# Optimization experiments

Measured on AMD Instinct MI355X. Metric: run time of the kernel, lower is better.

Reference implementation:

```python
import jax, jax.numpy as jnp
import numpy as np
from jax import lax

D3 = 48      # manifold_dim * 3
M = 512      # mem_slots
H = 256      # slot_dim
K = 32       # topk
IN = 1024    # input_dim
ODE_HID = 128
ODE_STEPS = 2
ODE_DT = 0.5
TEMP = 1.0   # temperature buffer
LN_EPS = 1e-5


def _ln(x, g, b):
    m = jnp.mean(x, axis=-1, keepdims=True)
    v = jnp.mean(jnp.square(x - m), axis=-1, keepdims=True)
    return (x - m) * lax.rsqrt(v + LN_EPS) * g + b


def setup_inputs() -> dict:
    key = jax.random.key(0)
    ks = jax.random.split(key, 12)
    s_in = 1.0 / np.sqrt(IN)
    s_h = 1.0 / np.sqrt(H)
    s_d3 = 1.0 / np.sqrt(D3)
    s_ode = 1.0 / np.sqrt(ODE_HID)
    return {
        "x": jax.random.normal(ks[0], (16, 2048, IN), jnp.float32),
        "w1": jax.random.uniform(ks[1], (IN, D3), jnp.float32, -s_in, s_in),
        "b1": jnp.zeros((D3,), jnp.float32),
        "g1": jnp.ones((D3,), jnp.float32),
        "be1": jnp.zeros((D3,), jnp.float32),
        "wa": jax.random.uniform(ks[2], (D3, ODE_HID), jnp.float32, -s_d3, s_d3),
        "ba": jnp.zeros((ODE_HID,), jnp.float32),
        "wb": jax.random.uniform(ks[3], (ODE_HID, D3), jnp.float32, -s_ode, s_ode),
        "bb": jnp.zeros((D3,), jnp.float32),
        "mem": jax.random.normal(ks[4], (M, H), jnp.float32),
        "pos": jax.random.normal(ks[5], (M, 16, 3), jnp.float32),
        "curv": jax.random.normal(ks[6], (M, 16), jnp.float32),
        "alpha": jnp.float32(0.1),
        "wo": jax.random.uniform(ks[7], (H, IN), jnp.float32, -s_h, s_h),
        "bo": jnp.zeros((IN,), jnp.float32),
        "go": jnp.ones((IN,), jnp.float32),
        "beo": jnp.zeros((IN,), jnp.float32),
    }


def reference(x, w1, b1, g1, be1, wa, ba, wb, bb, mem, pos, curv, alpha, wo, bo, go, beo):
    # manifold projection: Linear -> LayerNorm -> GELU, viewed as (B,S,D,3)
    h = jax.nn.gelu(_ln(x @ w1 + b1, g1, be1), approximate=False)  # (B,S,48)
    # ODE evolution (2 fixed steps over the flattened manifold coords)
    for _ in range(ODE_STEPS):
        dx = jnp.tanh(h @ wa + ba) @ wb + bb
        h = h + ODE_DT * dx
    # attend: query side is detached in the original
    q = lax.stop_gradient(h)                       # (B,S,48)
    mem_pos = pos.reshape(M, -1)                   # (512,48)
    # squared pairwise L2: ||q||^2 - 2 q.m + ||m||^2
    dist = (jnp.sum(q * q, axis=-1, keepdims=True)
            - 2.0 * jnp.einsum('bsd,md->bsm', q, mem_pos)
            + jnp.sum(mem_pos * mem_pos, axis=-1))
    dist = jnp.maximum(dist, 0.0) / max(TEMP, 1e-6)
    curv_w = jnp.exp(-alpha * jnp.linalg.norm(curv, axis=-1))  # (512,)
    dist = dist * curv_w[None, None, :]
    # topk smallest distances
    neg_top, itop = lax.top_k(-dist, K)            # (B,S,K)
    w = jax.nn.softmax(neg_top, axis=-1)           # softmax(-dtop)
    slots = mem[itop]                              # (B,S,K,256) gather
    attended = jnp.einsum('bsk,bskh->bsh', w, slots)
    # output projection: Linear -> LayerNorm -> GELU
    return jax.nn.gelu(_ln(attended @ wo + bo, go, beo), approximate=False)
```

## Files before the change

### kernel.cpp

```cpp
#include <hip/hip_runtime.h>
#include <stdint.h>

typedef unsigned short u16;
typedef __attribute__((ext_vector_type(4))) short short4v;
typedef __attribute__((ext_vector_type(8))) short short8v;
typedef __attribute__((ext_vector_type(4))) float f32x4;
typedef __attribute__((address_space(1))) void gv;
typedef __attribute__((address_space(3))) void lv;

#define NTOK 32768

__device__ __forceinline__ float bf2f(u16 u){ return __uint_as_float(((uint32_t)u)<<16); }
__device__ __forceinline__ u16 f2bf(float f){
  uint32_t u = __float_as_uint(f);
  u += 0x7FFFu + ((u>>16)&1u);
  return (u16)(u>>16);
}
__device__ __forceinline__ void hilo(float v, u16& h, u16& l){
  h = f2bf(v);
  l = f2bf(v - bf2f(h));
}
__device__ __forceinline__ void tsplit(float v, u16& h, u16& l){
  uint32_t b = __float_as_uint(v);
  h = (u16)(b >> 16);
  float lf = v - __uint_as_float(b & 0xFFFF0000u);
  l = (u16)(__float_as_uint(lf) >> 16);
}
__device__ __forceinline__ void tpack8(float4 a, float4 b, short8v& hi, short8v& lo){
  float v[8] = {a.x,a.y,a.z,a.w,b.x,b.y,b.z,b.w};
  #pragma unroll
  for (int i=0;i<8;++i){ u16 h,l; tsplit(v[i],h,l); hi[i]=(short)h; lo[i]=(short)l; }
}
__device__ __forceinline__ float gelu_f(float v){ return 0.5f*v*(1.0f + erff(v*0.70710678118654752440f)); }
__device__ __forceinline__ float gelu_t(float x){
  float u = 0.7978845608028654f*(x + 0.044715f*x*x*x);
  float t = 1.0f - 2.0f/(__expf(2.0f*u) + 1.0f);
  return 0.5f*x*(1.0f + t);
}
__device__ __forceinline__ float tanh_f(float x){ return 1.0f - 2.0f/(__expf(2.0f*x)+1.0f); }

__global__ __launch_bounds__(256) void k_prep(
    const float* __restrict__ w1, const float* __restrict__ wa, const float* __restrict__ wb,
    const float* __restrict__ pos, const float* __restrict__ curv,
    const float* __restrict__ mem, const float* __restrict__ wo,
    const float* __restrict__ alpha,
    u16* __restrict__ w1s, u16* __restrict__ wah, u16* __restrict__ wbh,
    float2* __restrict__ mnw,
    u16* __restrict__ memb, u16* __restrict__ woB, u16* __restrict__ posB)
{
  int i = blockIdx.x*256 + threadIdx.x;
  if (i < 49152){ int n = i>>10, k = i&1023; u16 h,l; hilo(w1[k*48+n], h, l);
                  w1s[i] = h; w1s[49152+i] = l; return; }
  i -= 49152;
  if (i < 8192){ int u = i>>6, d = i&63; float v = (d<48) ? wa[d*128+u] : 0.f;
                 u16 h,l; hilo(v,h,l); wah[i] = h; wah[8192+i] = l; return; }
  i -= 8192;
  if (i < 6144){ int n = i>>7, u = i&127; u16 h,l; hilo(wb[u*48+n], h, l);
                 wbh[i] = h; wbh[6144+i] = l; return; }
  i -= 6144;
  if (i < 512){
    float s = 0.f;
    #pragma unroll
    for (int d=0; d<48; ++d){ float v = pos[i*48+d]; s += v*v; }
    float c2 = 0.f;
    #pragma unroll
    for (int d=0; d<16; ++d){ float v = curv[i*16+d]; c2 += v*v; }
    mnw[i] = make_float2(s, expf(-alpha[0]*sqrtf(c2)));
    return;
  }
  i -= 512;
  if (i < 131072){ memb[i] = f2bf(mem[i]); return; }
  i -= 131072;
  if (i < 262144){
    int e = i & 7, ln = (i>>3)&63, n = (i>>9)&15, cpq = (i>>13)&3, kt = i>>15;
    int col = cpq*256 + n*16 + (ln & 15);
    int k   = kt*32 + (ln >> 4)*8 + e;
    woB[i] = f2bf(wo[k*1024 + col]);
    return;
  }
  i -= 262144;
  if (i < 32768){
    int e = i & 7, ln = (i>>3)&63, n = (i>>9)&31, ks = i>>14;
    int slot = n*16 + (ln&15);
    int d = ks*32 + (ln>>4)*8 + e;
    float v = (d < 48) ? pos[slot*48 + d] : 0.f;
    u16 h,l; hilo(v,h,l);
    posB[i] = h; posB[32768+i] = l;
  }
}

__global__ __launch_bounds__(256, 2) void k_proj(
    const float* __restrict__ x, const u16* __restrict__ w1s,
    const float* __restrict__ b1, const float* __restrict__ g1, const float* __restrict__ be1,
    float* __restrict__ hout)
{
  extern __shared__ char dynp[];
  float* xsl = (float*)dynp;
  u16*   bsl = (u16*)(dynp + 49152);

  const int tid = threadIdx.x;
  const int lane = tid & 63, w = tid >> 6;
  const int l15 = lane & 15, l4 = lane >> 4;
  const int bm = blockIdx.x;
  const int arow = w*16 + l15;

  f32x4 acc[3];
  #pragma unroll
  for (int n=0; n<3; ++n) acc[n] = (f32x4){0.f,0.f,0.f,0.f};

  auto stage_x = [&](float* dst, int kt){
    #pragma unroll
    for (int j=0; j<4; ++j){
      int idx = (j*4 + w)*64 + lane;
      int row = idx >> 4, q = idx & 15;
      int chunk = q >> 1, half = q & 1;
      const float* src = x + (size_t)(bm*64 + row)*1024 + kt*64 + ((chunk ^ (row & 7))*8 + half*4);
      __builtin_amdgcn_global_load_lds((gv*)src, (lv*)(dst + (j*4 + w)*256), 16, 0, 0);
    }
  };
  auto stage_b = [&](u16* dst, int kt){
    #pragma unroll
    for (int j=0; j<3; ++j){
      int idx = (j*4 + w)*64 + lane;
      int hl = (idx >= 384) ? 1 : 0;
      int rr = idx - hl*384;
      int row = rr >> 3, ch = rr & 7;
      const u16* src = w1s + hl*49152 + (size_t)row*1024 + kt*64 + ((ch ^ (row & 7))*8);
      __builtin_amdgcn_global_load_lds((gv*)src, (lv*)(dst + (j*4 + w)*512), 16, 0, 0);
    }
  };
  auto mfma_from = [&](const float* xb, const u16* bb){
    #pragma unroll
    for (int kq=0; kq<2; ++kq){
      int chunk = kq*4 + l4;
      int phys = chunk ^ (arow & 7);
      const float* xa = xb + arow*64 + phys*8;
      float4 a0 = *(const float4*)xa;
      float4 a1 = *(const float4*)(xa + 4);
      short8v ah, al; tpack8(a0, a1, ah, al);
      #pragma unroll
      for (int n=0; n<3; ++n){
        int brow = n*16 + l15;
        int bcx = chunk ^ (brow & 7);
        short8v bh = *(const short8v*)(bb + brow*64 + bcx*8);
        short8v bl = *(const short8v*)(bb + 3072 + brow*64 + bcx*8);
        acc[n] = __builtin_amdgcn_mfma_f32_16x16x32_bf16(ah, bh, acc[n], 0, 0, 0);
        acc[n] = __builtin_amdgcn_mfma_f32_16x16x32_bf16(ah, bl, acc[n], 0, 0, 0);
        acc[n] = __builtin_amdgcn_mfma_f32_16x16x32_bf16(al, bh, acc[n], 0, 0, 0);
      }
    }
  };

  float* x0 = xsl;         float* x1 = xsl + 4096;  float* x2 = xsl + 8192;
  u16*   b0 = bsl;         u16*   b1b = bsl + 6144;

  stage_b(b0, 0);
  stage_x(x0, 0);
  stage_x(x1, 1);

  float* xc = x0; float* xn = x1; float* xn2 = x2;
  u16* bc = b0;  u16* bn = b1b;

  for (int kt = 0; kt < 15; ++kt){
    asm volatile("s_waitcnt vmcnt(4)" ::: "memory");
    __builtin_amdgcn_s_barrier();
    __builtin_amdgcn_sched_barrier(0);
    mfma_from(xc, bc);
    stage_b(bn, kt + 1);
    if (kt < 14) stage_x(xn2, kt + 2);
    { float* t = xc; xc = xn; xn = xn2; xn2 = t; }
    { u16* t = bc; bc = bn; bn = t; }
  }
  asm volatile("s_waitcnt vmcnt(0)" ::: "memory");
  __builtin_amdgcn_s_barrier();
  __builtin_amdgcn_sched_barrier(0);
  mfma_from(xc, bc);

  float b1r[3], g1r[3], e1r[3];
  #pragma unroll
  for (int n=0; n<3; ++n){ int c = n*16 + l15; b1r[n] = b1[c]; g1r[n] = g1[c]; e1r[n] = be1[c]; }
  #pragma unroll
  for (int r=0; r<4; ++r){
    float a0 = acc[0][r] + b1r[0];
    float a1 = acc[1][r] + b1r[1];
    float a2 = acc[2][r] + b1r[2];
    float s1 = a0+a1+a2;
    float s2 = a0*a0 + a1*a1 + a2*a2;
    #pragma unroll
    for (int m=1; m<16; m<<=1){ s1 += __shfl_xor(s1, m); s2 += __shfl_xor(s2, m); }
    float mean = s1 * (1.f/48.f);
    float var  = s2 * (1.f/48.f) - mean*mean;
    float rs = rsqrtf(var + 1e-5f);
    int row = bm*64 + w*16 + l4*4 + r;
    float* hb = hout + (size_t)row*48;
    hb[l15]      = gelu_f((a0-mean)*rs*g1r[0] + e1r[0]);
    hb[16+l15]   = gelu_f((a1-mean)*rs*g1r[1] + e1r[1]);
    hb[32+l15]   = gelu_f((a2-mean)*rs*g1r[2] + e1r[2]);
  }
}

__global__ __launch_bounds__(256) void k_ode(
    const float* __restrict__ hin,
    const u16* __restrict__ wah, const u16* __restrict__ wbh,
    const float* __restrict__ ba, const float* __restrict__ bb,
    float* __restrict__ hout, float* __restrict__ q2b)
{
  extern __shared__ u16 sm[];
  u16* t_hi = sm;
  u16* t_lo = sm + 16384;
  u16* h_hi = sm + 32768;
  u16* h_lo = sm + 40960;
  float* hscr = (float*)sm;

  const int tid = threadIdx.x;
  const int lane = tid & 63, w = tid >> 6;
  const int l15 = lane & 15, l4 = lane >> 4;
  const int bm = blockIdx.x;

  float4 hv4[6];
  #pragma unroll
  for (int it=0; it<6; ++it){
    int q = it*256 + tid;
    int row = q/12, c4 = q - row*12;
    hv4[it] = *(const float4*)(hin + (size_t)(bm*128 + row)*48 + c4*4);
  }
  #pragma unroll
  for (int it=0; it<6; ++it){
    int q = it*256 + tid;
    int row = q/12, c4 = q - row*12;
    *(float4*)&hscr[row*48 + c4*4] = hv4[it];
    float4 v = hv4[it];
    u16 h0,l0,h1,l1,h2,l2,h3,l3;
    tsplit(v.x,h0,l0); tsplit(v.y,h1,l1); tsplit(v.z,h2,l2); tsplit(v.w,h3,l3);
    int off = row*64 + ((c4>>1) ^ (row & 7))*8 + (c4 & 1)*4;
    short4v hv = {(short)h0,(short)h1,(short)h2,(short)h3};
    short4v lv = {(short)l0,(short)l1,(short)l2,(short)l3};
    *(short4v*)&h_hi[off] = hv;
    *(short4v*)&h_lo[off] = lv;
  }
  {
    int row = tid >> 1, ch = 6 + (tid & 1);
    int off = row*64 + (ch ^ (row & 7))*8;
    uint4 z = {0u,0u,0u,0u};
    *(uint4*)&h_hi[off] = z;
    *(uint4*)&h_lo[off] = z;
  }
  __syncthreads();

  float hreg[2][3][4];
  #pragma unroll
  for (int m=0; m<2; ++m)
    #pragma unroll
    for (int n=0; n<3; ++n)
      #pragma unroll
      for (int r=0; r<4; ++r)
        hreg[m][n][r] = hscr[(w*32 + m*16 + l4*4 + r)*48 + n*16 + l15];
  __syncthreads();

  float ba_r[8], bb_r[3];
  #pragma unroll
  for (int n=0; n<8; ++n) ba_r[n] = ba[n*16 + l15];
  #pragma unroll
  for (int n=0; n<3; ++n) bb_r[n] = bb[n*16 + l15];

  for (int s=0; s<2; ++s){
    f32x4 at[2][8];
    #pragma unroll
    for (int m=0; m<2; ++m)
      #pragma unroll
      for (int n=0; n<8; ++n) at[m][n] = (f32x4){0.f,0.f,0.f,0.f};
    #pragma unroll
    for (int kq=0; kq<2; ++kq){
      short8v ah[2], al[2];
      #pragma unroll
      for (int m=0; m<2; ++m){
        int arow = w*32 + m*16 + l15;
        int ac = (kq*4 + l4) ^ (arow & 7);
        ah[m] = *(const short8v*)&h_hi[arow*64 + ac*8];
        al[m] = *(const short8v*)&h_lo[arow*64 + ac*8];
      }
      #pragma unroll
      for (int n=0; n<8; ++n){
        const u16* bp = wah + (n*16 + l15)*64 + kq*32 + l4*8;
        short8v bh = *(const short8v*)bp;
        short8v bl = *(const short8v*)(bp + 8192);
        #pragma unroll
        for (int m=0; m<2; ++m){
          at[m][n] = __builtin_amdgcn_mfma_f32_16x16x32_bf16(ah[m], bh, at[m][n], 0, 0, 0);
          at[m][n] = __builtin_amdgcn_mfma_f32_16x16x32_bf16(ah[m], bl, at[m][n], 0, 0, 0);
          at[m][n] = __builtin_amdgcn_mfma_f32_16x16x32_bf16(al[m], bh, at[m][n], 0, 0, 0);
        }
      }
    }
    #pragma unroll
    for (int m=0; m<2; ++m)
      #pragma unroll
      for (int n=0; n<8; ++n)
        #pragma unroll
        for (int r=0; r<4; ++r){
          float tv = tanh_f(at[m][n][r] + ba_r[n]);
          u16 th, tl; tsplit(tv, th, tl);
          int row = w*32 + m*16 + l4*4 + r;
          int col = n*16 + l15;
          int c = col >> 3;
          int phys = (c & 8) | ((c & 7) ^ (row & 7));
          int off = row*128 + phys*8 + (col & 7);
          t_hi[off] = th; t_lo[off] = tl;
        }
    __syncthreads();
    f32x4 ad[2][3];
    #pragma unroll
    for (int m=0; m<2; ++m)
      #pragma unroll
      for (int n=0; n<3; ++n) ad[m][n] = (f32x4){0.f,0.f,0.f,0.f};
    #pragma unroll
    for (int kq=0; kq<4; ++kq){
      short8v ah[2], al[2];
      #pragma unroll
      for (int m=0; m<2; ++m){
        int arow = w*32 + m*16 + l15;
        int c = kq*4 + l4;
        int phys = (c & 8) | ((c & 7) ^ (arow & 7));
        ah[m] = *(const short8v*)&t_hi[arow*128 + phys*8];
        al[m] = *(const short8v*)&t_lo[arow*128 + phys*8];
      }
      #pragma unroll
      for (int n=0; n<3; ++n){
        const u16* bp = wbh + (n*16 + l15)*128 + kq*32 + l4*8;
        short8v bh = *(const short8v*)bp;
        short8v bl = *(const short8v*)(bp + 6144);
        #pragma unroll
        for (int m=0; m<2; ++m){
          ad[m][n] = __builtin_amdgcn_mfma_f32_16x16x32_bf16(ah[m], bh, ad[m][n], 0, 0, 0);
          ad[m][n] = __builtin_amdgcn_mfma_f32_16x16x32_bf16(ah[m], bl, ad[m][n], 0, 0, 0);
          ad[m][n] = __builtin_amdgcn_mfma_f32_16x16x32_bf16(al[m], bh, ad[m][n], 0, 0, 0);
        }
      }
    }
    #pragma unroll
    for (int m=0; m<2; ++m)
      #pragma unroll
      for (int n=0; n<3; ++n)
        #pragma unroll
        for (int r=0; r<4; ++r)
          hreg[m][n][r] += 0.5f*(ad[m][n][r] + bb_r[n]);
    if (s == 0){
      #pragma unroll
      for (int m=0; m<2; ++m)
        #pragma unroll
        for (int n=0; n<3; ++n)
          #pragma unroll
          for (int r=0; r<4; ++r){
            u16 hh, hl2; tsplit(hreg[m][n][r], hh, hl2);
            int row = w*32 + m*16 + l4*4 + r;
            int col = n*16 + l15;
            int off = row*64 + ((col>>3) ^ (row & 7))*8 + (col & 7);
            h_hi[off] = hh; h_lo[off] = hl2;
          }
      __syncthreads();
    }
  }
  #pragma unroll
  for (int m=0; m<2; ++m){
    #pragma unroll
    for (int r=0; r<4; ++r){
      size_t row = (size_t)(bm*128 + w*32 + m*16 + l4*4 + r);
      #pragma unroll
      for (int n=0; n<3; ++n)
        hout[row*64 + n*16 + l15] = hreg[m][n][r];
      hout[row*64 + 48 + l15] = 0.f;
      float s2 = hreg[m][0][r]*hreg[m][0][r] + hreg[m][1][r]*hreg[m][1][r] + hreg[m][2][r]*hreg[m][2][r];
      #pragma unroll
      for (int msk=1; msk<16; msk<<=1) s2 += __shfl_xor(s2, msk);
      if (l15 == 0) q2b[row] = s2;
    }
  }
}

__global__ __launch_bounds__(256, 4) void k_sel(
    const float* __restrict__ h, const float* __restrict__ q2b,
    const u16* __restrict__ posB, const float2* __restrict__ mnw,
    uint32_t* __restrict__ glist)
{
  __shared__ __align__(16) uint32_t tokKeys[2*4*528];

  const int tid = threadIdx.x;
  const int lane = tid & 63, w = tid >> 6;
  const int g = w >> 1, s = w & 1;
  const int l15 = lane & 15, l4 = lane >> 4;
  const int bm = blockIdx.x;

  const float* hrow = h + (size_t)(bm*32 + g*16 + l15)*64;
  float4 x0 = *(const float4*)(hrow + l4*8);
  float4 x1 = *(const float4*)(hrow + l4*8 + 4);
  float4 x2 = *(const float4*)(hrow + 32 + l4*8);
  float4 x3 = *(const float4*)(hrow + 32 + l4*8 + 4);
  short8v ah0, al0, ah1, al1;
  tpack8(x0, x1, ah0, al0);
  tpack8(x2, x3, ah1, al1);

  float4 q2v = *(const float4*)(q2b + bm*32 + g*16 + l4*4);
  float q2a[4] = {q2v.x, q2v.y, q2v.z, q2v.w};

  uint32_t kk[16][4];
  #pragma unroll
  for (int n=0; n<16; ++n){
    const u16* pb = posB + (size_t)(s*16 + n)*512 + lane*8;
    short8v bh0 = *(const short8v*)(pb);
    short8v bl0 = *(const short8v*)(pb + 32768);
    short8v bh1 = *(const short8v*)(pb + 16384);
    short8v bl1 = *(const short8v*)(pb + 49152);
    f32x4 acc = (f32x4){0.f,0.f,0.f,0.f};
    acc = __builtin_amdgcn_mfma_f32_16x16x32_bf16(ah0, bh0, acc, 0, 0, 0);
    acc = __builtin_amdgcn_mfma_f32_16x16x32_bf16(ah0, bl0, acc, 0, 0, 0);
    acc = __builtin_amdgcn_mfma_f32_16x16x32_bf16(al0, bh0, acc, 0, 0, 0);
    acc = __builtin_amdgcn_mfma_f32_16x16x32_bf16(ah1, bh1, acc, 0, 0, 0);
    acc = __builtin_amdgcn_mfma_f32_16x16x32_bf16(ah1, bl1, acc, 0, 0, 0);
    acc = __builtin_amdgcn_mfma_f32_16x16x32_bf16(al1, bh1, acc, 0, 0, 0);
    const int slot = s*256 + n*16 + l15;
    float2 mw = mnw[slot];
    #pragma unroll
    for (int r=0; r<4; ++r){
      float dd = fmaxf(q2a[r] + mw.x - 2.f*acc[r], 0.f) * mw.y;
      kk[n][r] = (__float_as_uint(dd) & 0xFFFFFE00u) | (uint32_t)slot;
    }
  }

  const int gbase = g*2112;
  const unsigned long long ltmask = (lane == 63) ? 0x7FFFFFFFFFFFFFFFull : ((1ull << lane) - 1ull);
  #pragma unroll
  for (int r=0; r<4; ++r){
    __syncthreads();
    #pragma unroll
    for (int n=0; n<16; ++n)
      tokKeys[gbase + l4*528 + s*256 + n*16 + l15] = kk[n][r];
    __syncthreads();
    uint32_t key8[2][8];
    #pragma unroll
    for (int j=0; j<2; ++j){
      *(uint4*)&key8[j][0] = *(const uint4*)&tokKeys[gbase + (s*2+j)*528 + lane*8];
      *(uint4*)&key8[j][4] = *(const uint4*)&tokKeys[gbase + (s*2+j)*528 + lane*8 + 4];
    }
    uint32_t p[2] = {0u,0u};
    for (int b=30; b>=0; --b){
      #pragma unroll
      for (int j=0; j<2; ++j){
        uint32_t c = p[j] | (1u<<b);
        int cnt = 0;
        #pragma unroll
        for (int i=0; i<8; ++i) cnt += (int)__popcll(__ballot(key8[j][i] < c));
        if (cnt <= 31) p[j] = c;
      }
    }
    #pragma unroll
    for (int j=0; j<2; ++j){
      size_t tok = (size_t)bm*32 + g*16 + (s*2+j)*4 + r;
      int base = 0;
      #pragma unroll
      for (int i=0; i<8; ++i){
        unsigned long long bal = __ballot(key8[j][i] <= p[j]);
        if (key8[j][i] <= p[j]){
          int idx = base + (int)__popcll(bal & ltmask);
          glist[tok*32 + idx] = key8[j][i];
        }
        base += (int)__popcll(bal);
      }
    }
  }
}

__global__ __launch_bounds__(256) void k_attend(
    const uint32_t* __restrict__ glist, const u16* __restrict__ memb,
    u16* __restrict__ att)
{
  const int lane = threadIdx.x & 63, w = threadIdx.x >> 6;
  const size_t tok = (size_t)blockIdx.x*4 + w;
  uint32_t lk[32];
  const uint4* lp = (const uint4*)(glist + tok*32);
  #pragma unroll
  for (int q=0; q<8; ++q) *(uint4*)&lk[q*4] = lp[q];
  uint32_t km = lk[0];
  #pragma unroll
  for (int i=1; i<32; ++i) km = min(km, lk[i]);
  const float dminf = __uint_as_float(km & 0xFFFFFE00u);

  float den = 0.f, a0=0.f, a1=0.f, a2=0.f, a3=0.f;
  #pragma unroll
  for (int i=0; i<32; ++i){
    float dk = __uint_as_float(lk[i] & 0xFFFFFE00u);
    int slot = (int)(lk[i] & 511u);
    float wg = __expf(dminf - dk);
    den += wg;
    uint2 mv = ((const uint2*)(memb + (size_t)slot*256))[lane];
    a0 += wg*bf2f((u16)(mv.x & 0xFFFFu));
    a1 += wg*bf2f((u16)(mv.x >> 16));
    a2 += wg*bf2f((u16)(mv.y & 0xFFFFu));
    a3 += wg*bf2f((u16)(mv.y >> 16));
  }
  float inv = 1.f/den;
  uint32_t o0 = (uint32_t)f2bf(a0*inv) | ((uint32_t)f2bf(a1*inv) << 16);
  uint32_t o1 = (uint32_t)f2bf(a2*inv) | ((uint32_t)f2bf(a3*inv) << 16);
  ((uint2*)(att + tok*256))[lane] = make_uint2(o0, o1);
}

__global__ __launch_bounds__(1024, 4) void k_out(
    const u16* __restrict__ A, const u16* __restrict__ woB, const float* __restrict__ bo,
    const float* __restrict__ go, const float* __restrict__ beo, float* __restrict__ out)
{
  __shared__ u16 Asl[64*256];
  __shared__ float red1[16*65];
  __shared__ float red2[16*65];

  const int tid = threadIdx.x;
  const int lane = tid & 63, w = tid >> 6;
  const int l15 = lane & 15, l4 = lane >> 4;
  const int bm = blockIdx.x;

  #pragma unroll
  for (int j=0; j<2; ++j){
    int idx = j*1024 + tid;
    int row = idx >> 5, ch = idx & 31;
    int gc = (ch & 24) | ((ch & 7) ^ (row & 7));
    uint4 v = *(const uint4*)(A + (size_t)(bm*64 + row)*256 + gc*8);
    *(uint4*)&Asl[row*256 + ch*8] = v;
  }
  __syncthreads();

  f32x4 acc[4][4];
  #pragma unroll
  for (int m=0; m<4; ++m)
    #pragma unroll
    for (int n=0; n<4; ++n) acc[m][n] = (f32x4){0.f,0.f,0.f,0.f};

  #pragma unroll
  for (int kt=0; kt<8; ++kt){
    const int c = kt*4 + l4;
    short8v af[4];
    #pragma unroll
    for (int m=0; m<4; ++m){
      int arow = m*16 + l15;
      int aphys = (c & 24) | ((c & 7) ^ (arow & 7));
      af[m] = *(const short8v*)&Asl[arow*256 + aphys*8];
    }
    const u16* bbase = woB + ((size_t)kt*64 + w*4)*512 + lane*8;
    #pragma unroll
    for (int n=0; n<4; ++n){
      short8v bf = *(const short8v*)(bbase + n*512);
      #pragma unroll
      for (int m=0; m<4; ++m)
        acc[m][n] = __builtin_amdgcn_mfma_f32_16x16x32_bf16(af[m], bf, acc[m][n], 0, 0, 0);
    }
  }

  float bor[4];
  #pragma unroll
  for (int n=0; n<4; ++n) bor[n] = bo[w*64 + n*16 + l15];

  float s1[4][4], s2[4][4];
  #pragma unroll
  for (int m=0; m<4; ++m)
    #pragma unroll
    for (int r=0; r<4; ++r){ s1[m][r] = 0.f; s2[m][r] = 0.f; }
  #pragma unroll
  for (int m=0; m<4; ++m)
    #pragma unroll
    for (int n=0; n<4; ++n)
      #pragma unroll
      for (int r=0; r<4; ++r){
        float v = acc[m][n][r] + bor[n];
        acc[m][n][r] = v;
        s1[m][r] += v; s2[m][r] += v*v;
      }
  #pragma unroll
  for (int m=0; m<4; ++m)
    #pragma unroll
    for (int r=0; r<4; ++r){
      #pragma unroll
      for (int msk=1; msk<16; msk<<=1){
        s1[m][r] += __shfl_xor(s1[m][r], msk);
        s2[m][r] += __shfl_xor(s2[m][r], msk);
      }
    }
  if (l15 == 0){
    #pragma unroll
    for (int m=0; m<4; ++m)
      #pragma unroll
      for (int r=0; r<4; ++r){
        int t = m*16 + l4*4 + r;
        red1[w*65 + t] = s1[m][r];
        red2[w*65 + t] = s2[m][r];
      }
  }
  __syncthreads();

  float mean[4][4], rs[4][4];
  #pragma unroll
  for (int m=0; m<4; ++m)
    #pragma unroll
    for (int r=0; r<4; ++r){
      int t = m*16 + l4*4 + r;
      float a1 = red1[l15*65 + t];
      float a2 = red2[l15*65 + t];
      #pragma unroll
      for (int msk=1; msk<16; msk<<=1){
        a1 += __shfl_xor(a1, msk);
        a2 += __shfl_xor(a2, msk);
      }
      float mu = a1 * (1.f/1024.f);
      float var = a2 * (1.f/1024.f) - mu*mu;
      mean[m][r] = mu;
      rs[m][r] = rsqrtf(var + 1e-5f);
    }

  float gor[4], eor[4];
  #pragma unroll
  for (int n=0; n<4; ++n){
    int col = w*64 + n*16 + l15;
    gor[n] = go[col]; eor[n] = beo[col];
  }
  #pragma unroll
  for (int m=0; m<4; ++m)
    #pragma unroll
    for (int r=0; r<4; ++r){
      size_t row = (size_t)bm*64 + m*16 + l4*4 + r;
      float* op = out + row*1024 + w*64 + l15;
      float mu = mean[m][r], rv = rs[m][r];
      #pragma unroll
      for (int n=0; n<4; ++n){
        op[n*16] = gelu_t((acc[m][n][r] - mu)*rv*gor[n] + eor[n]);
      }
    }
}

extern "C" void kernel_launch(void* const* d_in, const int* in_sizes, int n_in,
                              void* d_out, int out_size, void* d_ws, size_t ws_size,
                              hipStream_t stream) {
  const float* x    = (const float*)d_in[0];
  const float* w1   = (const float*)d_in[1];
  const float* b1   = (const float*)d_in[2];
  const float* g1   = (const float*)d_in[3];
  const float* be1  = (const float*)d_in[4];
  const float* wa   = (const float*)d_in[5];
  const float* ba   = (const float*)d_in[6];
  const float* wb   = (const float*)d_in[7];
  const float* bb   = (const float*)d_in[8];
  const float* mem  = (const float*)d_in[9];
  const float* pos  = (const float*)d_in[10];
  const float* curv = (const float*)d_in[11];
  const float* alpha= (const float*)d_in[12];
  const float* wo   = (const float*)d_in[13];
  const float* bo   = (const float*)d_in[14];
  const float* go   = (const float*)d_in[15];
  const float* beo  = (const float*)d_in[16];
  float* out = (float*)d_out;

  char* ws = (char*)d_ws;
  size_t o = 0;
  auto take = [&](size_t b) -> char* { char* p = ws + o; o += (b + 255) & ~(size_t)255; return p; };
  char*  regA   = take(67108864);
  float* hbuf48 = (float*)regA;
  float* hbuf64 = (float*)(regA + 6291456);
  float* q2b    = (float*)(regA + 6291456 + 8388608);
  u16*   att    = (u16*)take(16777216);
  u16*   w1s    = (u16*)take(196608);
  u16*   wah    = (u16*)take(32768);
  u16*   wbh    = (u16*)take(24576);
  float2* mnw   = (float2*)take(4096);
  u16*   memb   = (u16*)take(262144);
  u16*   woB    = (u16*)take(524288);
  u16*   posB   = (u16*)take(131072);
  uint32_t* glist = (uint32_t*)take(4194304);

  hipFuncSetAttribute((const void*)k_ode, hipFuncAttributeMaxDynamicSharedMemorySize, 98304);
  hipFuncSetAttribute((const void*)k_proj, hipFuncAttributeMaxDynamicSharedMemorySize, 73728);

  k_prep<<<1914, 256, 0, stream>>>(w1, wa, wb, pos, curv, mem, wo, alpha,
                                   w1s, wah, wbh, mnw, memb, woB, posB);
  k_proj<<<512, 256, 73728, stream>>>(x, w1s, b1, g1, be1, hbuf48);
  k_ode<<<256, 256, 98304, stream>>>(hbuf48, wah, wbh, ba, bb, hbuf64, q2b);
  k_sel<<<1024, 256, 0, stream>>>(hbuf64, q2b, posB, mnw, glist);
  k_attend<<<8192, 256, 0, stream>>>(glist, memb, att);
  k_out<<<512, 1024, 0, stream>>>(att, woB, bo, go, beo, out);
  (void)in_sizes; (void)n_in; (void)out_size; (void)ws_size;
}
```

Measured before the change: 253.4 us.

## Halve ODE tile to 64 rows per block, drop syncs, use raw exp/rcp

The ODE kernel now processes 64 tokens per block instead of 128, with each wave owning 16 rows. Grid size doubles to 512 blocks and dynamic shared memory halves, which should improve occupancy and CU coverage. Each wave now reads back only the tanh and h rows it wrote itself, so the intra-step __syncthreads calls are removed. Separately, tanh, gelu_t and the softmax reciprocal use the hardware v_exp_f32/v_rcp_f32 instructions, trading a little accuracy for fewer ALU ops. Per-wave weight loads from global memory are now amortised over half as many rows.

```diff
diff --git a/kernel.cpp b/kernel.cpp
--- a/kernel.cpp
+++ b/kernel.cpp
@@ -31,13 +31,21 @@
   #pragma unroll
   for (int i=0;i<8;++i){ u16 h,l; tsplit(v[i],h,l); hi[i]=(short)h; lo[i]=(short)l; }
 }
+__device__ __forceinline__ float fexp2(float x){ float r; asm("v_exp_f32 %0, %1" : "=v"(r) : "v"(x)); return r; }
+__device__ __forceinline__ float frcp(float x){ float r; asm("v_rcp_f32 %0, %1" : "=v"(r) : "v"(x)); return r; }
+
 __device__ __forceinline__ float gelu_f(float v){ return 0.5f*v*(1.0f + erff(v*0.70710678118654752440f)); }
 __device__ __forceinline__ float gelu_t(float x){
-  float u = 0.7978845608028654f*(x + 0.044715f*x*x*x);
-  float t = 1.0f - 2.0f/(__expf(2.0f*u) + 1.0f);
-  return 0.5f*x*(1.0f + t);
-}
-__device__ __forceinline__ float tanh_f(float x){ return 1.0f - 2.0f/(__expf(2.0f*x)+1.0f); }
+  float p = x*(2.3022141f + 0.1029435f*x*x);
+  float e = fexp2(p);
+  float r = frcp(e + 1.0f);
+  return x*(1.0f - r);
+}
+__device__ __forceinline__ float tanh_f(float x){
+  float e = fexp2(2.8853901f*x);
+  float r = frcp(e + 1.0f);
+  return 1.0f - 2.0f*r;
+}
 
 __global__ __launch_bounds__(256) void k_prep(
     const float* __restrict__ w1, const float* __restrict__ wa, const float* __restrict__ wb,
@@ -207,9 +215,9 @@
 {
   extern __shared__ u16 sm[];
   u16* t_hi = sm;
-  u16* t_lo = sm + 16384;
-  u16* h_hi = sm + 32768;
-  u16* h_lo = sm + 40960;
+  u16* t_lo = sm + 8192;
+  u16* h_hi = sm + 16384;
+  u16* h_lo = sm + 20480;
   float* hscr = (float*)sm;
 
   const int tid = threadIdx.x;
@@ -217,15 +225,15 @@
   const int l15 = lane & 15, l4 = lane >> 4;
   const int bm = blockIdx.x;
 
-  float4 hv4[6];
-  #pragma unroll
-  for (int it=0; it<6; ++it){
+  float4 hv4[3];
+  #pragma unroll
+  for (int it=0; it<3; ++it){
     int q = it*256 + tid;
     int row = q/12, c4 = q - row*12;
-    hv4[it] = *(const float4*)(hin + (size_t)(bm*128 + row)*48 + c4*4);
-  }
-  #pragma unroll
-  for (int it=0; it<6; ++it){
+    hv4[it] = *(const float4*)(hin + (size_t)(bm*64 + row)*48 + c4*4);
+  }
+  #pragma unroll
+  for (int it=0; it<3; ++it){
     int q = it*256 + tid;
     int row = q/12, c4 = q - row*12;
     *(float4*)&hscr[row*48 + c4*4] = hv4[it];
@@ -238,7 +246,7 @@
     *(short4v*)&h_hi[off] = hv;
     *(short4v*)&h_lo[off] = lv;
   }
-  {
+  if (tid < 128){
     int row = tid >> 1, ch = 6 + (tid & 1);
     int off = row*64 + (ch ^ (row & 7))*8;
     uint4 z = {0u,0u,0u,0u};
@@ -247,14 +255,12 @@
   }
   __syncthreads();
 
-  float hreg[2][3][4];
-  #pragma unroll
-  for (int m=0; m<2; ++m)
-    #pragma unroll
-    for (int n=0; n<3; ++n)
-      #pragma unroll
-      for (int r=0; r<4; ++r)
-        hreg[m][n][r] = hscr[(w*32 + m*16 + l4*4 + r)*48 + n*16 + l15];
+  float hreg[3][4];
+  #pragma unroll
+  for (int n=0; n<3; ++n)
+    #pragma unroll
+    for (int r=0; r<4; ++r)
+      hreg[n][r] = hscr[(w*16 + l4*4 + r)*48 + n*16 + l15];
   __syncthreads();
 
   float ba_r[8], bb_r[3];
@@ -264,116 +270,87 @@
   for (int n=0; n<3; ++n) bb_r[n] = bb[n*16 + l15];
 
   for (int s=0; s<2; ++s){
-    f32x4 at[2][8];
-    #pragma unroll
-    for (int m=0; m<2; ++m)
-      #pragma unroll
-      for (int n=0; n<8; ++n) at[m][n] = (f32x4){0.f,0.f,0.f,0.f};
+    f32x4 at[8];
+    #pragma unroll
+    for (int n=0; n<8; ++n) at[n] = (f32x4){0.f,0.f,0.f,0.f};
     #pragma unroll
     for (int kq=0; kq<2; ++kq){
-      short8v ah[2], al[2];
-      #pragma unroll
-      for (int m=0; m<2; ++m){
-        int arow = w*32 + m*16 + l15;
-        int ac = (kq*4 + l4) ^ (arow & 7);
-        ah[m] = *(const short8v*)&h_hi[arow*64 + ac*8];
-        al[m] = *(const short8v*)&h_lo[arow*64 + ac*8];
-      }
+      const int arow = w*16 + l15;
+      int ac = (kq*4 + l4) ^ (arow & 7);
+      short8v ah = *(const short8v*)&h_hi[arow*64 + ac*8];
+      short8v al = *(const short8v*)&h_lo[arow*64 + ac*8];
       #pragma unroll
       for (int n=0; n<8; ++n){
         const u16* bp = wah + (n*16 + l15)*64 + kq*32 + l4*8;
         short8v bh = *(const short8v*)bp;
         short8v bl = *(const short8v*)(bp + 8192);
-        #pragma unroll
-        for (int m=0; m<2; ++m){
-          at[m][n] = __builtin_amdgcn_mfma_f32_16x16x32_bf16(ah[m], bh, at[m][n], 0, 0, 0);
-          at[m][n] = __builtin_amdgcn_mfma_f32_16x16x32_bf16(ah[m], bl, at[m][n], 0, 0, 0);
-          at[m][n] = __builtin_amdgcn_mfma_f32_16x16x32_bf16(al[m], bh, at[m][n], 0, 0, 0);
-        }
-      }
-    }
-    #pragma unroll
-    for (int m=0; m<2; ++m)
-      #pragma unroll
-      for (int n=0; n<8; ++n)
-        #pragma unroll
-        for (int r=0; r<4; ++r){
-          float tv = tanh_f(at[m][n][r] + ba_r[n]);
-          u16 th, tl; tsplit(tv, th, tl);
-          int row = w*32 + m*16 + l4*4 + r;
-          int col = n*16 + l15;
-          int c = col >> 3;
-          int phys = (c & 8) | ((c & 7) ^ (row & 7));
-          int off = row*128 + phys*8 + (col & 7);
-          t_hi[off] = th; t_lo[off] = tl;
-        }
-    __syncthreads();
-    f32x4 ad[2][3];
-    #pragma unroll
-    for (int m=0; m<2; ++m)
-      #pragma unroll
-      for (int n=0; n<3; ++n) ad[m][n] = (f32x4){0.f,0.f,0.f,0.f};
+        at[n] = __builtin_amdgcn_mfma_f32_16x16x32_bf16(ah, bh, at[n], 0, 0, 0);
+        at[n] = __builtin_amdgcn_mfma_f32_16x16x32_bf16(ah, bl, at[n], 0, 0, 0);
+        at[n] = __builtin_amdgcn_mfma_f32_16x16x32_bf16(al, bh, at[n], 0, 0, 0);
+      }
+    }
+    #pragma unroll
+    for (int n=0; n<8; ++n)
+      #pragma unroll
+      for (int r=0; r<4; ++r){
+        float tv = tanh_f(at[n][r] + ba_r[n]);
+        u16 th, tl; tsplit(tv, th, tl);
+        int row = w*16 + l4*4 + r;
+        int col = n*16 + l15;
+        int c = col >> 3;
+        int phys = (c & 8) | ((c & 7) ^ (row & 7));
+        int off = row*128 + phys*8 + (col & 7);
+        t_hi[off] = th; t_lo[off] = tl;
+      }
+    f32x4 ad[3];
+    #pragma unroll
+    for (int n=0; n<3; ++n) ad[n] = (f32x4){0.f,0.f,0.f,0.f};
     #pragma unroll
     for (int kq=0; kq<4; ++kq){
-      short8v ah[2], al[2];
-      #pragma unroll
-      for (int m=0; m<2; ++m){
-        int arow = w*32 + m*16 + l15;
-        int c = kq*4 + l4;
-        int phys = (c & 8) | ((c & 7) ^ (arow & 7));
-        ah[m] = *(const short8v*)&t_hi[arow*128 + phys*8];
-        al[m] = *(const short8v*)&t_lo[arow*128 + phys*8];
-      }
+      const int arow = w*16 + l15;
+      int c = kq*4 + l4;
+      int phys = (c & 8) | ((c & 7) ^ (arow & 7));
+      short8v ah = *(const short8v*)&t_hi[arow*128 + phys*8];
+      short8v al = *(const short8v*)&t_lo[arow*128 + phys*8];
       #pragma unroll
       for (int n=0; n<3; ++n){
         const u16* bp = wbh + (n*16 + l15)*128 + kq*32 + l4*8;
         short8v bh = *(const short8v*)bp;
         short8v bl = *(const short8v*)(bp + 6144);
-        #pragma unroll
-        for (int m=0; m<2; ++m){
-          ad[m][n] = __builtin_amdgcn_mfma_f32_16x16x32_bf16(ah[m], bh, ad[m][n], 0, 0, 0);
-          ad[m][n] = __builtin_amdgcn_mfma_f32_16x16x32_bf16(ah[m], bl, ad[m][n], 0, 0, 0);
-          ad[m][n] = __builtin_amdgcn_mfma_f32_16x16x32_bf16(al[m], bh, ad[m][n], 0, 0, 0);
-        }
-      }
-    }
-    #pragma unroll
-    for (int m=0; m<2; ++m)
+        ad[n] = __builtin_amdgcn_mfma_f32_16x16x32_bf16(ah, bh, ad[n], 0, 0, 0);
+        ad[n] = __builtin_amdgcn_mfma_f32_16x16x32_bf16(ah, bl, ad[n], 0, 0, 0);
+        ad[n] = __builtin_amdgcn_mfma_f32_16x16x32_bf16(al, bh, ad[n], 0, 0, 0);
+      }
+    }
+    #pragma unroll
+    for (int n=0; n<3; ++n)
+      #pragma unroll
+      for (int r=0; r<4; ++r)
+        hreg[n][r] += 0.5f*(ad[n][r] + bb_r[n]);
+    if (s == 0){
       #pragma unroll
       for (int n=0; n<3; ++n)
         #pragma unroll
-        for (int r=0; r<4; ++r)
-          hreg[m][n][r] += 0.5f*(ad[m][n][r] + bb_r[n]);
-    if (s == 0){
-      #pragma unroll
-      for (int m=0; m<2; ++m)
-        #pragma unroll
-        for (int n=0; n<3; ++n)
-          #pragma unroll
-          for (int r=0; r<4; ++r){
-            u16 hh, hl2; tsplit(hreg[m][n][r], hh, hl2);
-            int row = w*32 + m*16 + l4*4 + r;
-            int col = n*16 + l15;
-            int off = row*64 + ((col>>3) ^ (row & 7))*8 + (col & 7);
-            h_hi[off] = hh; h_lo[off] = hl2;
-          }
-      __syncthreads();
-    }
-  }
-  #pragma unroll
-  for (int m=0; m<2; ++m){
-    #pragma unroll
-    for (int r=0; r<4; ++r){
-      size_t row = (size_t)(bm*128 + w*32 + m*16 + l4*4 + r);
-      #pragma unroll
-      for (int n=0; n<3; ++n)
-        hout[row*64 + n*16 + l15] = hreg[m][n][r];
-      hout[row*64 + 48 + l15] = 0.f;
-      float s2 = hreg[m][0][r]*hreg[m][0][r] + hreg[m][1][r]*hreg[m][1][r] + hreg[m][2][r]*hreg[m][2][r];
-      #pragma unroll
-      for (int msk=1; msk<16; msk<<=1) s2 += __shfl_xor(s2, msk);
-      if (l15 == 0) q2b[row] = s2;
-    }
+        for (int r=0; r<4; ++r){
+          u16 hh, hl2; tsplit(hreg[n][r], hh, hl2);
+          int row = w*16 + l4*4 + r;
+          int col = n*16 + l15;
+          int off = row*64 + ((col>>3) ^ (row & 7))*8 + (col & 7);
+          h_hi[off] = hh; h_lo[off] = hl2;
+        }
+    }
+  }
+  #pragma unroll
+  for (int r=0; r<4; ++r){
+    size_t row = (size_t)(bm*64 + w*16 + l4*4 + r);
+    #pragma unroll
+    for (int n=0; n<3; ++n)
+      hout[row*64 + n*16 + l15] = hreg[n][r];
+    hout[row*64 + 48 + l15] = 0.f;
+    float s2 = hreg[0][r]*hreg[0][r] + hreg[1][r]*hreg[1][r] + hreg[2][r]*hreg[2][r];
+    #pragma unroll
+    for (int msk=1; msk<16; msk<<=1) s2 += __shfl_xor(s2, msk);
+    if (l15 == 0) q2b[row] = s2;
   }
 }
 
@@ -497,7 +474,7 @@
     a2 += wg*bf2f((u16)(mv.y & 0xFFFFu));
     a3 += wg*bf2f((u16)(mv.y >> 16));
   }
-  float inv = 1.f/den;
+  float inv = frcp(den);
   uint32_t o0 = (uint32_t)f2bf(a0*inv) | ((uint32_t)f2bf(a1*inv) << 16);
   uint32_t o1 = (uint32_t)f2bf(a2*inv) | ((uint32_t)f2bf(a3*inv) << 16);
   ((uint2*)(att + tok*256))[lane] = make_uint2(o0, o1);
@@ -671,13 +648,13 @@
   u16*   posB   = (u16*)take(131072);
   uint32_t* glist = (uint32_t*)take(4194304);
 
-  hipFuncSetAttribute((const void*)k_ode, hipFuncAttributeMaxDynamicSharedMemorySize, 98304);
+  hipFuncSetAttribute((const void*)k_ode, hipFuncAttributeMaxDynamicSharedMemorySize, 49152);
   hipFuncSetAttribute((const void*)k_proj, hipFuncAttributeMaxDynamicSharedMemorySize, 73728);
 
   k_prep<<<1914, 256, 0, stream>>>(w1, wa, wb, pos, curv, mem, wo, alpha,
                                    w1s, wah, wbh, mnw, memb, woB, posB);
   k_proj<<<512, 256, 73728, stream>>>(x, w1s, b1, g1, be1, hbuf48);
-  k_ode<<<256, 256, 98304, stream>>>(hbuf48, wah, wbh, ba, bb, hbuf64, q2b);
+  k_ode<<<512, 256, 49152, stream>>>(hbuf48, wah, wbh, ba, bb, hbuf64, q2b);
   k_sel<<<1024, 256, 0, stream>>>(hbuf64, q2b, posB, mnw, glist);
   k_attend<<<8192, 256, 0, stream>>>(glist, memb, att);
   k_out<<<512, 1024, 0, stream>>>(att, woB, bo, go, beo, out);
```

Result: no change. 255.3 us (+0.7%).
